# Kernel tuning notes

Hardware: AMD Instinct MI355X
Metric: run time of the kernel (lower is better)

The kernel has to match this reference:

```python
import jax, jax.numpy as jnp
import numpy as np

TEMP = 0.07  # temperature used as logits / 0.07 in the original


def setup_inputs() -> dict:
    key = jax.random.key(0)
    k1, k2, k3 = jax.random.split(key, 3)
    B, N, T, L, D = 8, 128, 8, 6, 256
    meta = jax.random.normal(k1, (B, N, T, L, D), dtype=jnp.float32)
    thing = jax.random.randint(k2, (B, N, T), 0, 2, dtype=jnp.int32)
    label = jax.random.randint(k3, (B, N, T), 0, 40, dtype=jnp.int32)
    return {"meta_weight_for_con": meta, "thing_gt_idx": thing, "label_tmp": label}


def _con_loss(meta, thing, label):
    # meta: [B,N,T,L,D]; thing,label: [B,N,T]
    B, N, T, L, D = meta.shape
    P = N * T
    valid = thing.reshape(B, P).astype(bool)            # [B,P] boolean gt mask
    lab = label.reshape(B, P)                           # [B,P]
    # meta_weight_b[mask] -> [K,L,D]; permute(1,0,2) -> per-layer [K,D].
    # We keep all P positions and mask instead of compacting (jit-friendly).
    w = meta.reshape(B, P, L, D).transpose(0, 2, 1, 3)  # [B,L,P,D]
    w = w / jnp.maximum(jnp.linalg.norm(w, axis=-1, keepdims=True), 1e-12)  # F.normalize
    z = jnp.einsum('blpd,blqd->blpq', w, w) / TEMP      # similarity / temp [B,L,P,P]

    same = lab[:, :, None] == lab[:, None, :]           # [B,P,P]
    vpair = valid[:, :, None] & valid[:, None, :]
    eye = jnp.eye(P, dtype=bool)
    pos_mask = same & (~eye) & vpair                    # positives: same label, not self
    neg_mask = (~same) & vpair                          # negatives: different label

    K = valid.sum(axis=1)                               # [B] ins_num_ per batch
    pos_count = pos_mask.sum(axis=-1)                   # [B,P]
    neg_count = neg_mask.sum(axis=-1)                   # [B,P]

    # --- random positive sample per (batch, layer, row), mirroring np.random.choice ---
    u = jax.random.uniform(jax.random.key(42), (B, L, P))
    r = jnp.floor(u * pos_count[:, None, :].astype(u.dtype)).astype(jnp.int32)
    r = jnp.minimum(r, jnp.maximum(pos_count - 1, 0)[:, None, :])
    ranks = jnp.cumsum(pos_mask, axis=-1) - 1           # rank of each positive in index order
    sel = pos_mask[:, None, :, :] & (ranks[:, None, :, :] == r[..., None])  # [B,L,P,P]
    zp = jnp.sum(jnp.where(sel, z, 0.0), axis=-1)       # chosen positive logit [B,L,P]
    diag = jnp.diagonal(z, axis1=-2, axis2=-1)          # self-sim fallback when no positives
    zp = jnp.where((pos_count > 0)[:, None, :], zp, diag)

    # --- last negative (original pads by repeating the last negative to K-1) ---
    iota = jnp.arange(P)
    idx_last = jnp.max(jnp.where(neg_mask, iota[None, None, :], -1), axis=-1)  # [B,P]
    idx = jnp.broadcast_to(jnp.maximum(idx_last, 0)[:, None, :, None], (B, L, P, 1))
    zl = jnp.take_along_axis(z, idx, axis=-1)[..., 0]   # [B,L,P]

    # --- stable CE with label 0: loss = lse(logits) - zp ---
    max_n = jnp.max(jnp.where(neg_mask[:, None], z, -jnp.inf), axis=-1)  # [B,L,P]
    m = jnp.maximum(zp, max_n)
    m = jnp.where(jnp.isfinite(m), m, zp)
    sum_neg = jnp.sum(jnp.where(neg_mask[:, None], jnp.exp(z - m[..., None]), 0.0), axis=-1)
    pad = jnp.maximum((K[:, None] - 1 - neg_count), 0).astype(z.dtype)   # [B,P]
    pad_term = pad[:, None, :] * jnp.where((neg_count > 0)[:, None, :], jnp.exp(zl - m), 0.0)
    loss_row = m + jnp.log(jnp.exp(zp - m) + sum_neg + pad_term) - zp    # [B,L,P]

    row_w = valid.astype(z.dtype)
    mean_per = jnp.sum(loss_row * row_w[:, None, :], axis=-1) / jnp.maximum(K, 1)[:, None].astype(z.dtype)  # [B,L]

    gate = jnp.sum((thing.sum(axis=2) > 0), axis=1) >= 2  # skip batches with <2 gt rows
    return jnp.sum(jnp.where(gate[:, None], mean_per, 0.0))


def reference(meta_weight_for_con, thing_gt_idx, label_tmp):
    return _con_loss(meta_weight_for_con, thing_gt_idx, label_tmp)
```

## Files before the change

kernel.cpp:

```cpp
#include <hip/hip_runtime.h>
#include <stdint.h>

namespace {

constexpr int Bb = 8, Ll = 6, Dd = 256, Pp = 1024;
constexpr float SCALE_Y = 14.285714285714286f * 1.4426950408889634f;
constexpr float M0y = 21.0f;
constexpr float LN2f = 0.6931471805599453f;

typedef __attribute__((ext_vector_type(4))) float floatx4;

__device__ const int PAIRS[36] = {
  0x00,0x01,0x02,0x03,0x04,0x05,0x06,0x07,
  0x11,0x12,0x13,0x14,0x15,0x16,0x17,
  0x22,0x23,0x24,0x25,0x26,0x27,
  0x33,0x34,0x35,0x36,0x37,
  0x44,0x45,0x46,0x47,
  0x55,0x56,0x57,
  0x66,0x67,
  0x77
};

__device__ __forceinline__ void async16(const void* g, void* l) {
  __builtin_amdgcn_global_load_lds(
      (const __attribute__((address_space(1))) void*)g,
      (__attribute__((address_space(3))) void*)l, 16, 0, 0);
}

__device__ __forceinline__ uint32_t rotl32(uint32_t x, int n) {
  return (x << n) | (x >> (32 - n));
}
__device__ __forceinline__ void tf_round(uint32_t& x0, uint32_t& x1, int r) {
  x0 += x1; x1 = rotl32(x1, r); x1 ^= x0;
}
__device__ void threefry2x32(uint32_t x0, uint32_t x1, uint32_t& o0, uint32_t& o1) {
  const uint32_t k0 = 0u, k1 = 42u;
  const uint32_t k2 = k0 ^ k1 ^ 0x1BD11BDAu;
  x0 += k0; x1 += k1;
  tf_round(x0,x1,13); tf_round(x0,x1,15); tf_round(x0,x1,26); tf_round(x0,x1,6);
  x0 += k1; x1 += k2 + 1u;
  tf_round(x0,x1,17); tf_round(x0,x1,29); tf_round(x0,x1,16); tf_round(x0,x1,24);
  x0 += k2; x1 += k0 + 2u;
  tf_round(x0,x1,13); tf_round(x0,x1,15); tf_round(x0,x1,26); tf_round(x0,x1,6);
  x0 += k0; x1 += k1 + 3u;
  tf_round(x0,x1,17); tf_round(x0,x1,29); tf_round(x0,x1,16); tf_round(x0,x1,24);
  x0 += k1; x1 += k2 + 4u;
  tf_round(x0,x1,13); tf_round(x0,x1,15); tf_round(x0,x1,26); tf_round(x0,x1,6);
  x0 += k2; x1 += k0 + 5u;
  o0 = x0; o1 = x1;
}
__device__ float jax_u01(uint32_t idx) {
  const uint32_t HALF = (uint32_t)(Bb * Ll * Pp / 2);
  uint32_t o0, o1, bits;
  if (idx < HALF) { threefry2x32(idx, idx + HALF, o0, o1); bits = o0; }
  else            { threefry2x32(idx - HALF, idx, o0, o1); bits = o1; }
  return __uint_as_float((bits >> 9) | 0x3f800000u) - 1.0f;
}

__device__ __forceinline__ uint32_t fp8e4m3_rne(float x) {
  uint32_t u = __float_as_uint(x);
  const uint32_t s = (u >> 24) & 0x80u;
  u &= 0x7FFFFFFFu;
  uint32_t code;
  if (u < 0x3C800000u) {
    code = (uint32_t)__float2int_rn(__uint_as_float(u) * 512.0f);
  } else {
    const uint32_t r = (u + 0x7FFFFu + ((u >> 20) & 1u)) >> 20;
    code = r - (120u << 3);
  }
  return s | code;
}
__device__ __forceinline__ float fp8e4m3_tof(uint32_t c) {
  const uint32_t e = (c >> 3) & 15u, m = c & 7u;
  float mag;
  if (e) mag = __uint_as_float(((e + 120u) << 23) | (m << 20));
  else   mag = (float)m * 0.001953125f;
  return (c & 0x80u) ? -mag : mag;
}

constexpr int NB_NORM = Bb * Pp * Ll / 4;
constexpr int NB_ROW  = Bb * Pp / 4;

__global__ void prep_k(const float* __restrict__ meta, const int* __restrict__ thing,
                       const int* __restrict__ label, uint8_t* __restrict__ wn,
                       int* __restrict__ qpos, int* __restrict__ negc,
                       int* __restrict__ qidx, int* __restrict__ Kv,
                       int* __restrict__ gatev, float* __restrict__ rowsum_g,
                       float* __restrict__ out) {
  __shared__ int sK[256], sG[256];
  const int bid = blockIdx.x, t = threadIdx.x;

  if (bid < NB_NORM) {
    const int wid = (bid * 256 + t) >> 6;
    const int lane = t & 63;
    const float4 v = *(const float4*)(meta + (size_t)wid * Dd + lane * 4);
    float ss = v.x * v.x + v.y * v.y + v.z * v.z + v.w * v.w;
    #pragma unroll
    for (int m = 32; m; m >>= 1) ss += __shfl_xor(ss, m, 64);
    const float inv = 1.0f / fmaxf(sqrtf(ss), 1e-12f);
    const int bp = wid / Ll, l = wid - bp * Ll;
    const int b = bp >> 10, p = bp & (Pp - 1);
    uint8_t* dst = wn + ((size_t)(b * Ll + l) * Pp + p) * Dd + lane * 4;
    const uint32_t packed = fp8e4m3_rne(v.x * inv)
                          | (fp8e4m3_rne(v.y * inv) << 8)
                          | (fp8e4m3_rne(v.z * inv) << 16)
                          | (fp8e4m3_rne(v.w * inv) << 24);
    *(uint32_t*)dst = packed;
    return;
  }
  if (bid < NB_NORM + NB_ROW) {
    const int wid = (bid - NB_NORM) * 4 + (t >> 6);
    const int lane = t & 63;
    const int b = wid >> 10, p = wid & (Pp - 1);
    const int* lab = label + b * Pp;
    const int* th  = thing + b * Pp;
    const int myLab = lab[p];
    const bool myValid = (th[p] != 0);

    uint32_t posbits = 0;
    int cnt[16];
    int pc = 0, nc = 0, last = -1;
    #pragma unroll
    for (int c = 0; c < 16; ++c) {
      const int q = c * 64 + lane;
      const int lq = lab[q];
      const bool vq = (th[q] != 0);
      const bool same = (lq == myLab);
      const bool pos = myValid && vq && same && (q != p);
      const bool neg = myValid && vq && !same;
      uint64_t bp2 = __ballot(pos);
      uint64_t bn = __ballot(neg);
      if (pos) posbits |= (1u << c);
      cnt[c] = __popcll(bp2);
      pc += cnt[c];
      nc += __popcll(bn);
      if (bn) last = c * 64 + 63 - __clzll(bn);
    }
    int qsel[Ll];
    #pragma unroll
    for (int l = 0; l < Ll; ++l) qsel[l] = p;
    if (pc > 0) {
      for (int l = 0; l < Ll; ++l) {
        const float u = jax_u01((uint32_t)((b * Ll + l) * Pp + p));
        int r = (int)floorf(u * (float)pc);
        r = min(r, pc - 1);
        int base = 0;
        for (int c = 0; c < 16; ++c) {
          if (r < base + cnt[c]) {
            const bool mine = (posbits >> c) & 1u;
            uint64_t bm = __ballot(mine);
            uint64_t ltmask = (lane == 0) ? 0ull : (~0ull >> (64 - lane));
            int myrank = __popcll(bm & ltmask);
            bool hit = mine && (base + myrank == r);
            uint64_t hb = __ballot(hit);
            qsel[l] = c * 64 + (int)__builtin_ctzll(hb);
            break;
          }
          base += cnt[c];
        }
      }
    }
    if (lane == 0) {
      negc[wid] = nc;
      qidx[wid] = (last < 0) ? 0 : last;
      #pragma unroll
      for (int l = 0; l < Ll; ++l) qpos[(b * Ll + l) * Pp + p] = qsel[l];
    }
    return;
  }
  if (bid < NB_NORM + NB_ROW + Bb) {
    const int b = bid - (NB_NORM + NB_ROW);
    int k = 0;
    for (int p = t; p < Pp; p += 256) k += (thing[b * Pp + p] != 0);
    int g = 0;
    if (t < 128) {
      int any = 0;
      for (int tt = 0; tt < 8; ++tt) any |= (thing[(b * 128 + t) * 8 + tt] != 0);
      g = any;
    }
    sK[t] = k; sG[t] = g;
    __syncthreads();
    for (int s = 128; s; s >>= 1) {
      if (t < s) { sK[t] += sK[t + s]; sG[t] += sG[t + s]; }
      __syncthreads();
    }
    if (t == 0) { Kv[b] = sK[0]; gatev[b] = (sG[0] >= 2) ? 1 : 0; }
    return;
  }
  if (bid < NB_NORM + NB_ROW + Bb + 48) {
    const int idx = (bid - (NB_NORM + NB_ROW + Bb)) * 256 + t;
    *(float4*)(rowsum_g + idx * 4) = (float4){0.f, 0.f, 0.f, 0.f};
    return;
  }
  if (t == 0) out[0] = 0.f;
}

__global__ void zpzl_k(const uint8_t* __restrict__ wn,
                       const int* __restrict__ qpos, const int* __restrict__ qidx,
                       float* __restrict__ zp_g, float* __restrict__ zl_g) {
  const int wid = blockIdx.x * 4 + (threadIdx.x >> 6);
  const int lane = threadIdx.x & 63;
  const int bl = wid >> 10, p = wid & (Pp - 1);
  const int b = bl / Ll;
  const int qp = qpos[bl * Pp + p];
  const int qi = qidx[b * Pp + p];
  const uint8_t* W = wn + (size_t)bl * Pp * Dd;
  const uint32_t a4 = *(const uint32_t*)(W + (size_t)p  * Dd + lane * 4);
  const uint32_t b4 = *(const uint32_t*)(W + (size_t)qp * Dd + lane * 4);
  const uint32_t c4 = *(const uint32_t*)(W + (size_t)qi * Dd + lane * 4);
  float sp = 0.f, sl = 0.f;
  #pragma unroll
  for (int i = 0; i < 4; ++i) {
    const float a = fp8e4m3_tof((a4 >> (8 * i)) & 0xFF);
    sp += a * fp8e4m3_tof((b4 >> (8 * i)) & 0xFF);
    sl += a * fp8e4m3_tof((c4 >> (8 * i)) & 0xFF);
  }
  #pragma unroll
  for (int m = 32; m; m >>= 1) {
    sp += __shfl_xor(sp, m, 64);
    sl += __shfl_xor(sl, m, 64);
  }
  if (lane == 0) {
    zp_g[bl * Pp + p] = sp * SCALE_Y;
    zl_g[bl * Pp + p] = sl * SCALE_Y;
  }
}

__global__ __launch_bounds__(256)
void gemm_loss_k(const uint8_t* __restrict__ wn,
                 const int* __restrict__ thing, const int* __restrict__ label,
                 float* __restrict__ rowsum_g) {
  __shared__ __align__(16) uint8_t As[128 * 128];
  __shared__ __align__(16) uint8_t Bs[128 * 128];
  __shared__ int labp_s[128], valp_s[128], labq_s[128], valq_s[128];
  __shared__ float rowsum_lds[128], colsum_lds[128];

  const int t = threadIdx.x;
  const int bid = blockIdx.x;
  const int xcd = bid & 7;
  const int chunk = bid >> 3;
  const int bl = xcd + 8 * (chunk % 6);
  const int b = bl / Ll;
  const int pair = PAIRS[chunk / 6];
  const int pt = pair >> 4, qt = pair & 15;
  const bool diag = (pt == qt);
  const int p0 = pt * 128, q0 = qt * 128;

  if (t < 128) {
    labp_s[t] = label[b * Pp + p0 + t];
    valp_s[t] = thing[b * Pp + p0 + t];
    labq_s[t] = label[b * Pp + q0 + t];
    valq_s[t] = thing[b * Pp + q0 + t];
    rowsum_lds[t] = 0.f;
    colsum_lds[t] = 0.f;
  }

  const uint8_t* Wbl = wn + (size_t)bl * Pp * Dd;
  const int lane = t & 63;
  const int w = t >> 6, wr = w >> 1, wc = w & 1;
  const int cq = lane & 15, rq = lane >> 4;
  const int wbase16 = (t & ~63) * 16;

  floatx4 acc[4][4];
  #pragma unroll
  for (int i = 0; i < 4; ++i)
    #pragma unroll
    for (int j = 0; j < 4; ++j) acc[i][j] = (floatx4){0.f, 0.f, 0.f, 0.f};

  const uint8_t* Bbase = diag ? As : Bs;

  for (int k0 = 0; k0 < Dd; k0 += 128) {
    __syncthreads();
    #pragma unroll
    for (int it = 0; it < 4; ++it) {
      const int c = it * 256 + t;
      const int row = c >> 3, sp = c & 7;
      const int sl = sp ^ (row & 7);
      async16(Wbl + (size_t)(p0 + row) * Dd + k0 + sl * 16, As + it * 4096 + wbase16);
      if (!diag)
        async16(Wbl + (size_t)(q0 + row) * Dd + k0 + sl * 16, Bs + it * 4096 + wbase16);
    }
    __syncthreads();
    #pragma unroll
    for (int sub = 0; sub < 4; ++sub) {
      const int Lw = sub * 2 + (rq >> 1);
      const int off8 = (rq & 1) * 8;
      long long af[4], bf[4];
      #pragma unroll
      for (int fi = 0; fi < 4; ++fi) {
        const int row = wr * 64 + fi * 16 + cq;
        af[fi] = *(const long long*)(As + row * 128 + (Lw ^ (row & 7)) * 16 + off8);
      }
      #pragma unroll
      for (int fj = 0; fj < 4; ++fj) {
        const int row = wc * 64 + fj * 16 + cq;
        bf[fj] = *(const long long*)(Bbase + row * 128 + (Lw ^ (row & 7)) * 16 + off8);
      }
      #pragma unroll
      for (int fi = 0; fi < 4; ++fi)
        #pragma unroll
        for (int fj = 0; fj < 4; ++fj)
          acc[fi][fj] = __builtin_amdgcn_mfma_f32_16x16x32_fp8_fp8(af[fi], bf[fj],
                                                                   acc[fi][fj], 0, 0, 0);
    }
  }

  int qlabv[4];
  float qvalf[4];
  float csum[4] = {0.f, 0.f, 0.f, 0.f};
  #pragma unroll
  for (int fj = 0; fj < 4; ++fj) {
    const int cl = wc * 64 + fj * 16 + cq;
    qlabv[fj] = labq_s[cl];
    qvalf[fj] = valq_s[cl] ? 1.f : 0.f;
  }
  #pragma unroll
  for (int fi = 0; fi < 4; ++fi) {
    #pragma unroll
    for (int reg = 0; reg < 4; ++reg) {
      const int rl = wr * 64 + fi * 16 + rq * 4 + reg;
      const int rlab = labp_s[rl];
      const float rvalf = valp_s[rl] ? 1.f : 0.f;
      float rsum = 0.f;
      #pragma unroll
      for (int fj = 0; fj < 4; ++fj) {
        const float y = acc[fi][fj][reg] * SCALE_Y;
        const float negm = (qlabv[fj] != rlab) ? (qvalf[fj] * rvalf) : 0.f;
        const float term = negm * exp2f(y - M0y);
        rsum += term;
        csum[fj] += term;
      }
      rsum += __shfl_xor(rsum, 1); rsum += __shfl_xor(rsum, 2);
      rsum += __shfl_xor(rsum, 4); rsum += __shfl_xor(rsum, 8);
      if (cq == 0) atomicAdd(&rowsum_lds[rl], rsum);
    }
  }
  if (!diag) {
    #pragma unroll
    for (int fj = 0; fj < 4; ++fj) {
      float c = csum[fj];
      c += __shfl_xor(c, 16); c += __shfl_xor(c, 32);
      if (rq == 0) atomicAdd(&colsum_lds[wc * 64 + fj * 16 + cq], c);
    }
  }
  __syncthreads();
  if (t < 128) {
    atomicAdd(&rowsum_g[bl * Pp + p0 + t], rowsum_lds[t]);
    if (!diag) atomicAdd(&rowsum_g[bl * Pp + q0 + t], colsum_lds[t]);
  }
}

__global__ void finalize_k(const float* __restrict__ rowsum_g, const float* __restrict__ zp_g,
                           const float* __restrict__ zl_g, const int* __restrict__ negc,
                           const int* __restrict__ thing, const int* __restrict__ Kv,
                           const int* __restrict__ gatev, float* __restrict__ out) {
  const int bl = blockIdx.x, b = bl / Ll, t = threadIdx.x;
  const int Kb = Kv[b];
  const float invK = 1.f / (float)max(Kb, 1);
  float acc = 0.f;
  for (int p = t; p < Pp; p += 256) {
    if (thing[b * Pp + p] != 0) {
      const float yp = zp_g[bl * Pp + p], yl = zl_g[bl * Pp + p];
      const float rs = rowsum_g[bl * Pp + p];
      const int nc = negc[b * Pp + p];
      const float pad = fmaxf((float)(Kb - 1 - nc), 0.f);
      const float tot = exp2f(yp - M0y) + rs + ((nc > 0) ? pad * exp2f(yl - M0y) : 0.f);
      acc += LN2f * (M0y + log2f(tot) - yp) * invK;
    }
  }
  __shared__ float sb[256];
  sb[t] = acc;
  __syncthreads();
  for (int s = 128; s; s >>= 1) {
    if (t < s) sb[t] += sb[t + s];
    __syncthreads();
  }
  if (t == 0 && gatev[b]) atomicAdd(out, sb[0]);
}

}

extern "C" void kernel_launch(void* const* d_in, const int* in_sizes, int n_in,
                              void* d_out, int out_size, void* d_ws, size_t ws_size,
                              hipStream_t stream) {
  const float* meta = (const float*)d_in[0];
  const int* thing  = (const int*)d_in[1];
  const int* label  = (const int*)d_in[2];
  float* out = (float*)d_out;

  char* ws = (char*)d_ws;
  size_t off = 0;
  uint8_t* wn = (uint8_t*)(ws + off); off += (size_t)Bb * Ll * Pp * Dd;
  int* qpos  = (int*)(ws + off); off += (size_t)Bb * Ll * Pp * 4;
  int* negc  = (int*)(ws + off); off += (size_t)Bb * Pp * 4;
  int* qidx  = (int*)(ws + off); off += (size_t)Bb * Pp * 4;
  int* Kv    = (int*)(ws + off); off += 64;
  int* gatev = (int*)(ws + off); off += 64;
  float* rowsum_g = (float*)(ws + off); off += (size_t)Bb * Ll * Pp * 4;
  float* zp_g     = (float*)(ws + off); off += (size_t)Bb * Ll * Pp * 4;
  float* zl_g     = (float*)(ws + off); off += (size_t)Bb * Ll * Pp * 4;

  const int nb_prep = NB_NORM + NB_ROW + Bb + 48 + 1;
  prep_k<<<nb_prep, 256, 0, stream>>>(meta, thing, label, wn, qpos, negc, qidx,
                                      Kv, gatev, rowsum_g, out);
  zpzl_k<<<(Bb * Ll * Pp) / 4, 256, 0, stream>>>(wn, qpos, qidx, zp_g, zl_g);
  gemm_loss_k<<<1728, 256, 0, stream>>>(wn, thing, label, rowsum_g);
  finalize_k<<<Bb * Ll, 256, 0, stream>>>(rowsum_g, zp_g, zl_g, negc, thing, Kv, gatev, out);
}
```

Baseline: 157.9 us.

## Fuse positive/last logit gathers into finalize, double-buffer GEMM, use hw fp8 converts

The separate zpzl kernel goes away and its gathered dot products are computed inside a wider finalize kernel. That removes one launch and the zp/zl global round trip, and lets gated-off batches skip all of the work. The GEMM now stages K in 64-wide chunks into double-buffered LDS, so the next tile's async loads overlap with the MFMAs on the current one. It uses a new swizzle and one barrier per step. Software fp8 encode and decode are replaced by the hardware cvt builtins when they are available, which may round slightly differently from the manual RNE path.

```diff
diff --git a/kernel.cpp b/kernel.cpp
--- a/kernel.cpp
+++ b/kernel.cpp
@@ -78,6 +78,20 @@
   return (c & 0x80u) ? -mag : mag;
 }
 
+__device__ __forceinline__ void fp8x4_tof(uint32_t u, float f[4]) {
+#if __has_builtin(__builtin_amdgcn_cvt_f32_fp8)
+  f[0] = __builtin_amdgcn_cvt_f32_fp8((int)u, 0);
+  f[1] = __builtin_amdgcn_cvt_f32_fp8((int)u, 1);
+  f[2] = __builtin_amdgcn_cvt_f32_fp8((int)u, 2);
+  f[3] = __builtin_amdgcn_cvt_f32_fp8((int)u, 3);
+#else
+  f[0] = fp8e4m3_tof(u & 0xFF);
+  f[1] = fp8e4m3_tof((u >> 8) & 0xFF);
+  f[2] = fp8e4m3_tof((u >> 16) & 0xFF);
+  f[3] = fp8e4m3_tof((u >> 24) & 0xFF);
+#endif
+}
+
 constexpr int NB_NORM = Bb * Pp * Ll / 4;
 constexpr int NB_ROW  = Bb * Pp / 4;
 
@@ -101,10 +115,16 @@
     const int bp = wid / Ll, l = wid - bp * Ll;
     const int b = bp >> 10, p = bp & (Pp - 1);
     uint8_t* dst = wn + ((size_t)(b * Ll + l) * Pp + p) * Dd + lane * 4;
+#if __has_builtin(__builtin_amdgcn_cvt_pk_fp8_f32)
+    const int lo16 = __builtin_amdgcn_cvt_pk_fp8_f32(v.x * inv, v.y * inv, 0, false);
+    const uint32_t packed =
+        (uint32_t)__builtin_amdgcn_cvt_pk_fp8_f32(v.z * inv, v.w * inv, lo16, true);
+#else
     const uint32_t packed = fp8e4m3_rne(v.x * inv)
                           | (fp8e4m3_rne(v.y * inv) << 8)
                           | (fp8e4m3_rne(v.z * inv) << 16)
                           | (fp8e4m3_rne(v.w * inv) << 24);
+#endif
     *(uint32_t*)dst = packed;
     return;
   }
@@ -195,43 +215,12 @@
   if (t == 0) out[0] = 0.f;
 }
 
-__global__ void zpzl_k(const uint8_t* __restrict__ wn,
-                       const int* __restrict__ qpos, const int* __restrict__ qidx,
-                       float* __restrict__ zp_g, float* __restrict__ zl_g) {
-  const int wid = blockIdx.x * 4 + (threadIdx.x >> 6);
-  const int lane = threadIdx.x & 63;
-  const int bl = wid >> 10, p = wid & (Pp - 1);
-  const int b = bl / Ll;
-  const int qp = qpos[bl * Pp + p];
-  const int qi = qidx[b * Pp + p];
-  const uint8_t* W = wn + (size_t)bl * Pp * Dd;
-  const uint32_t a4 = *(const uint32_t*)(W + (size_t)p  * Dd + lane * 4);
-  const uint32_t b4 = *(const uint32_t*)(W + (size_t)qp * Dd + lane * 4);
-  const uint32_t c4 = *(const uint32_t*)(W + (size_t)qi * Dd + lane * 4);
-  float sp = 0.f, sl = 0.f;
-  #pragma unroll
-  for (int i = 0; i < 4; ++i) {
-    const float a = fp8e4m3_tof((a4 >> (8 * i)) & 0xFF);
-    sp += a * fp8e4m3_tof((b4 >> (8 * i)) & 0xFF);
-    sl += a * fp8e4m3_tof((c4 >> (8 * i)) & 0xFF);
-  }
-  #pragma unroll
-  for (int m = 32; m; m >>= 1) {
-    sp += __shfl_xor(sp, m, 64);
-    sl += __shfl_xor(sl, m, 64);
-  }
-  if (lane == 0) {
-    zp_g[bl * Pp + p] = sp * SCALE_Y;
-    zl_g[bl * Pp + p] = sl * SCALE_Y;
-  }
-}
-
 __global__ __launch_bounds__(256)
 void gemm_loss_k(const uint8_t* __restrict__ wn,
                  const int* __restrict__ thing, const int* __restrict__ label,
                  float* __restrict__ rowsum_g) {
-  __shared__ __align__(16) uint8_t As[128 * 128];
-  __shared__ __align__(16) uint8_t Bs[128 * 128];
+  __shared__ __align__(16) uint8_t As[2 * 128 * 64];
+  __shared__ __align__(16) uint8_t Bs[2 * 128 * 64];
   __shared__ int labp_s[128], valp_s[128], labq_s[128], valq_s[128];
   __shared__ float rowsum_lds[128], colsum_lds[128];
 
@@ -267,42 +256,52 @@
     #pragma unroll
     for (int j = 0; j < 4; ++j) acc[i][j] = (floatx4){0.f, 0.f, 0.f, 0.f};
 
-  const uint8_t* Bbase = diag ? As : Bs;
-
-  for (int k0 = 0; k0 < Dd; k0 += 128) {
-    __syncthreads();
-    #pragma unroll
-    for (int it = 0; it < 4; ++it) {
-      const int c = it * 256 + t;
-      const int row = c >> 3, sp = c & 7;
-      const int sl = sp ^ (row & 7);
-      async16(Wbl + (size_t)(p0 + row) * Dd + k0 + sl * 16, As + it * 4096 + wbase16);
+  auto STAGE = [&](int bsel, int kt) {
+    const int k0 = kt * 64;
+    #pragma unroll
+    for (int rd = 0; rd < 2; ++rd) {
+      const int c = rd * 256 + t;
+      const int row = c >> 2, sp2 = c & 3;
+      const int sl = sp2 ^ ((row >> 1) & 3);
+      async16(Wbl + (size_t)(p0 + row) * Dd + k0 + sl * 16,
+              As + bsel * 8192 + rd * 4096 + wbase16);
       if (!diag)
-        async16(Wbl + (size_t)(q0 + row) * Dd + k0 + sl * 16, Bs + it * 4096 + wbase16);
-    }
-    __syncthreads();
-    #pragma unroll
-    for (int sub = 0; sub < 4; ++sub) {
+        async16(Wbl + (size_t)(q0 + row) * Dd + k0 + sl * 16,
+                Bs + bsel * 8192 + rd * 4096 + wbase16);
+    }
+  };
+
+  STAGE(0, 0);
+  __syncthreads();
+
+  for (int kt = 0; kt < 4; ++kt) {
+    const int bsel = kt & 1;
+    if (kt < 3) STAGE(bsel ^ 1, kt + 1);
+    const uint8_t* Ab = As + bsel * 8192;
+    const uint8_t* Bb2 = diag ? Ab : (Bs + bsel * 8192);
+    #pragma unroll
+    for (int sub = 0; sub < 2; ++sub) {
       const int Lw = sub * 2 + (rq >> 1);
       const int off8 = (rq & 1) * 8;
-      long long af[4], bf[4];
+      long long af[4], bfr[4];
       #pragma unroll
       for (int fi = 0; fi < 4; ++fi) {
         const int row = wr * 64 + fi * 16 + cq;
-        af[fi] = *(const long long*)(As + row * 128 + (Lw ^ (row & 7)) * 16 + off8);
+        af[fi] = *(const long long*)(Ab + row * 64 + (Lw ^ ((row >> 1) & 3)) * 16 + off8);
       }
       #pragma unroll
       for (int fj = 0; fj < 4; ++fj) {
         const int row = wc * 64 + fj * 16 + cq;
-        bf[fj] = *(const long long*)(Bbase + row * 128 + (Lw ^ (row & 7)) * 16 + off8);
+        bfr[fj] = *(const long long*)(Bb2 + row * 64 + (Lw ^ ((row >> 1) & 3)) * 16 + off8);
       }
       #pragma unroll
       for (int fi = 0; fi < 4; ++fi)
         #pragma unroll
         for (int fj = 0; fj < 4; ++fj)
-          acc[fi][fj] = __builtin_amdgcn_mfma_f32_16x16x32_fp8_fp8(af[fi], bf[fj],
+          acc[fi][fj] = __builtin_amdgcn_mfma_f32_16x16x32_fp8_fp8(af[fi], bfr[fj],
                                                                    acc[fi][fj], 0, 0, 0);
     }
+    __syncthreads();
   }
 
   int qlabv[4];
@@ -350,22 +349,51 @@
   }
 }
 
-__global__ void finalize_k(const float* __restrict__ rowsum_g, const float* __restrict__ zp_g,
-                           const float* __restrict__ zl_g, const int* __restrict__ negc,
-                           const int* __restrict__ thing, const int* __restrict__ Kv,
-                           const int* __restrict__ gatev, float* __restrict__ out) {
-  const int bl = blockIdx.x, b = bl / Ll, t = threadIdx.x;
-  const int Kb = Kv[b];
-  const float invK = 1.f / (float)max(Kb, 1);
+__global__ void final_k(const uint8_t* __restrict__ wn,
+                        const int* __restrict__ qpos, const int* __restrict__ qidx,
+                        const float* __restrict__ rowsum_g, const int* __restrict__ negc,
+                        const int* __restrict__ thing, const int* __restrict__ Kv,
+                        const int* __restrict__ gatev, float* __restrict__ out) {
+  const int t = threadIdx.x, lane = t & 63, wv = t >> 6;
+  const int bl = blockIdx.x >> 5;
+  const int b = bl / Ll;
+  const int p0 = (blockIdx.x & 31) * 32 + wv * 8;
   float acc = 0.f;
-  for (int p = t; p < Pp; p += 256) {
-    if (thing[b * Pp + p] != 0) {
-      const float yp = zp_g[bl * Pp + p], yl = zl_g[bl * Pp + p];
-      const float rs = rowsum_g[bl * Pp + p];
-      const int nc = negc[b * Pp + p];
-      const float pad = fmaxf((float)(Kb - 1 - nc), 0.f);
-      const float tot = exp2f(yp - M0y) + rs + ((nc > 0) ? pad * exp2f(yl - M0y) : 0.f);
-      acc += LN2f * (M0y + log2f(tot) - yp) * invK;
+  if (gatev[b]) {
+    const int Kb = Kv[b];
+    const float invK = 1.f / (float)max(Kb, 1);
+    const uint8_t* W = wn + (size_t)bl * Pp * Dd;
+    for (int i = 0; i < 8; ++i) {
+      const int p = p0 + i;
+      if (thing[b * Pp + p] == 0) continue;
+      const int qp = qpos[bl * Pp + p];
+      const int qi = qidx[b * Pp + p];
+      const uint32_t a4 = *(const uint32_t*)(W + (size_t)p  * Dd + lane * 4);
+      const uint32_t b4 = *(const uint32_t*)(W + (size_t)qp * Dd + lane * 4);
+      const uint32_t c4 = *(const uint32_t*)(W + (size_t)qi * Dd + lane * 4);
+      float fa[4], fb[4], fc[4];
+      fp8x4_tof(a4, fa);
+      fp8x4_tof(b4, fb);
+      fp8x4_tof(c4, fc);
+      float sp = 0.f, sl = 0.f;
+      #pragma unroll
+      for (int j = 0; j < 4; ++j) {
+        sp += fa[j] * fb[j];
+        sl += fa[j] * fc[j];
+      }
+      #pragma unroll
+      for (int m = 32; m; m >>= 1) {
+        sp += __shfl_xor(sp, m, 64);
+        sl += __shfl_xor(sl, m, 64);
+      }
+      if (lane == 0) {
+        const float yp = sp * SCALE_Y, yl = sl * SCALE_Y;
+        const float rs = rowsum_g[bl * Pp + p];
+        const int nc = negc[b * Pp + p];
+        const float pad = fmaxf((float)(Kb - 1 - nc), 0.f);
+        const float tot = exp2f(yp - M0y) + rs + ((nc > 0) ? pad * exp2f(yl - M0y) : 0.f);
+        acc += LN2f * (M0y + log2f(tot) - yp) * invK;
+      }
     }
   }
   __shared__ float sb[256];
@@ -375,7 +403,7 @@
     if (t < s) sb[t] += sb[t + s];
     __syncthreads();
   }
-  if (t == 0 && gatev[b]) atomicAdd(out, sb[0]);
+  if (t == 0 && sb[0] != 0.f) atomicAdd(out, sb[0]);
 }
 
 }
@@ -397,13 +425,10 @@
   int* Kv    = (int*)(ws + off); off += 64;
   int* gatev = (int*)(ws + off); off += 64;
   float* rowsum_g = (float*)(ws + off); off += (size_t)Bb * Ll * Pp * 4;
-  float* zp_g     = (float*)(ws + off); off += (size_t)Bb * Ll * Pp * 4;
-  float* zl_g     = (float*)(ws + off); off += (size_t)Bb * Ll * Pp * 4;
 
   const int nb_prep = NB_NORM + NB_ROW + Bb + 48 + 1;
   prep_k<<<nb_prep, 256, 0, stream>>>(meta, thing, label, wn, qpos, negc, qidx,
                                       Kv, gatev, rowsum_g, out);
-  zpzl_k<<<(Bb * Ll * Pp) / 4, 256, 0, stream>>>(wn, qpos, qidx, zp_g, zl_g);
   gemm_loss_k<<<1728, 256, 0, stream>>>(wn, thing, label, rowsum_g);
-  finalize_k<<<Bb * Ll, 256, 0, stream>>>(rowsum_g, zp_g, zl_g, negc, thing, Kv, gatev, out);
-}
+  final_k<<<1536, 256, 0, stream>>>(wn, qpos, qidx, rowsum_g, negc, thing, Kv, gatev, out);
+}
```

After: 163.2 us. 1.03x slower.
